# Kernel optimization log

Measured on AMD Instinct MI355X. Metric: run time of the kernel, lower is better.

## Reference

```python
import jax, jax.numpy as jnp
import numpy as np

B, H, L, D = 1, 8, 2048, 64
DP = 3   # positional coord dim
RE = 1   # extra relative features appended via concat
F = DP + RE  # LazyLinear in-features


def setup_inputs() -> dict:
    key = jax.random.key(0)
    ks = jax.random.split(key, 12)
    return {
        "q": jax.random.normal(ks[0], (B, H, L, D), jnp.float32),
        "k": jax.random.normal(ks[1], (B, H, L, D), jnp.float32),
        "v": jax.random.normal(ks[2], (B, H, L, D), jnp.float32),
        "c": jax.random.uniform(ks[3], (B, 1, 1, L), jnp.float32),
        "d_q": jax.random.normal(ks[4], (B, L, DP), jnp.float32),
        "d_k_top": jax.random.normal(ks[5], (B, L, DP), jnp.float32),
        "d_k_bot": jax.random.normal(ks[6], (B, L, DP), jnp.float32),
        "d_k_score": jax.random.uniform(ks[7], (B, L, 2, F), jnp.float32),
        "relative_top": jax.random.normal(ks[8], (B, L, L, RE), jnp.float32),
        "relative_bottom": jax.random.normal(ks[9], (B, L, L, RE), jnp.float32),
        "W_w": jax.random.normal(ks[10], (F, H), jnp.float32) * 0.1,
        "W_b": jax.random.normal(ks[11], (F, H), jnp.float32) * 0.1,
    }


def _pairwise_diff(a, b):
    # a: [B,Lq,Dp], b: [B,Lk,Dp] -> [B,Lq,Lk,Dp]
    return a[:, :, None, :] - b[:, None, :, :]


def reference(q, k, v, c, d_q, d_k_top, d_k_bot, d_k_score,
              relative_top, relative_bottom, W_w, W_b):
    # score function: scaled dot product -> [B,H,Lq,Lk]
    scores = jnp.einsum('bhqd,bhkd->bhqk', q, k) * (q.shape[-1] ** -0.5)

    # relative-position bias path
    dt = jnp.concatenate([_pairwise_diff(d_q, d_k_top), relative_top], axis=-1)     # [B,Lq,Lk,F]
    db = jnp.concatenate([_pairwise_diff(d_q, d_k_bot), relative_bottom], axis=-1)  # [B,Lq,Lk,F]
    dm = jnp.stack([dt, db], axis=3)                 # [B,Lq,Lk,2,F]
    dm = dm * d_k_score[:, None]                     # broadcast over Lq
    dm = dm.sum(axis=3)                              # [B,Lq,Lk,F]

    w = jax.nn.softplus(dm @ W_w).transpose(0, 3, 1, 2)  # [B,H,Lq,Lk]
    b = (dm @ W_b).transpose(0, 3, 1, 2)                 # [B,H,Lq,Lk]
    scores = scores * w + b

    # leaky probability function: softmax gated by per-key sampling weights c
    probs = jax.nn.softmax(scores, axis=-1) * c      # [B,H,Lq,Lk]

    out = jnp.einsum('bhqk,bhkd->bhqd', probs, v)
    return out, probs
```

## Files before the change

kernel.cpp:

```cpp
#include <hip/hip_runtime.h>
#include <cstdint>
#include <cstddef>

#define NH 8
#define LQ 2048
#define DH 64
#define NKT_Q 8

typedef __attribute__((ext_vector_type(8))) __bf16 bf16x8;
typedef __attribute__((ext_vector_type(8))) unsigned short ushort8;
typedef __attribute__((ext_vector_type(4))) float floatx4;

__device__ __forceinline__ unsigned short bf_trunc(float x) {
    return (unsigned short)(__float_as_uint(x) >> 16);
}
__device__ __forceinline__ float bf_up(unsigned short h) {
    return __uint_as_float(((unsigned int)h) << 16);
}
__device__ __forceinline__ unsigned short bf_rne(float x) {
    unsigned int u = __float_as_uint(x);
    return (unsigned short)((u + 0x7FFFu + ((u >> 16) & 1u)) >> 16);
}
struct hl_t { unsigned short h, l; };
__device__ __forceinline__ hl_t split2(float x) {
    hl_t r;
    r.h = bf_trunc(x);
    r.l = bf_trunc(x - bf_up(r.h));
    return r;
}

#define MFMA16(A, B, C) __builtin_amdgcn_mfma_f32_16x16x32_bf16((A), (B), (C), 0, 0, 0)

__global__ __launch_bounds__(256, 4) void attn_main(
    const float* __restrict__ qp,  const float* __restrict__ kp,
    const float* __restrict__ vp,  const float* __restrict__ cp,
    const float* __restrict__ dqp, const float* __restrict__ dktp,
    const float* __restrict__ dkbp,const float* __restrict__ dksp,
    const float* __restrict__ rtp, const float* __restrict__ rbp,
    const float* __restrict__ Wwp, const float* __restrict__ Wbp,
    float* __restrict__ probp, float* __restrict__ lws, float* __restrict__ pvws)
{
    __shared__ unsigned short sh_khi[64 * 72];
    __shared__ unsigned short sh_klo[64 * 72];
    __shared__ unsigned short sh_vhi[64 * 72];
    __shared__ unsigned short sh_vlo[64 * 72];
    __shared__ float sh_meta[64 * 13];
    __shared__ float sh_dqs[64 * 3];

    const int bid  = blockIdx.x;
    const int quar = bid & 3;
    const int h    = (bid >> 2) & 7;
    const int qt   = bid >> 5;
    const int q0   = qt * 64;
    const int t    = threadIdx.x;
    const int lane = t & 63;
    const int m    = lane & 15;
    const int quad = lane >> 4;
    const int w16  = (t >> 6) * 16;

    float Ww[4], Wb[4];
#pragma unroll
    for (int f = 0; f < 4; ++f) { Ww[f] = Wwp[f * NH + h]; Wb[f] = Wbp[f * NH + h]; }

    {
        const int row = t >> 2, s = t & 3;
        const float* src = qp + ((size_t)(h * LQ + q0 + row)) * DH + s * 16;
        ushort8 vh0, vh1, vl0, vl1;
#pragma unroll
        for (int j = 0; j < 2; ++j) {
            float4 x = *(const float4*)(src + 4 * j);
            hl_t a = split2(x.x * 0.125f), b = split2(x.y * 0.125f);
            hl_t c = split2(x.z * 0.125f), d = split2(x.w * 0.125f);
            vh0[4 * j + 0] = a.h; vl0[4 * j + 0] = a.l;
            vh0[4 * j + 1] = b.h; vl0[4 * j + 1] = b.l;
            vh0[4 * j + 2] = c.h; vl0[4 * j + 2] = c.l;
            vh0[4 * j + 3] = d.h; vl0[4 * j + 3] = d.l;
        }
#pragma unroll
        for (int j = 0; j < 2; ++j) {
            float4 x = *(const float4*)(src + 8 + 4 * j);
            hl_t a = split2(x.x * 0.125f), b = split2(x.y * 0.125f);
            hl_t c = split2(x.z * 0.125f), d = split2(x.w * 0.125f);
            vh1[4 * j + 0] = a.h; vl1[4 * j + 0] = a.l;
            vh1[4 * j + 1] = b.h; vl1[4 * j + 1] = b.l;
            vh1[4 * j + 2] = c.h; vl1[4 * j + 2] = c.l;
            vh1[4 * j + 3] = d.h; vl1[4 * j + 3] = d.l;
        }
        const int base = row * 72 + s * 16;
        *(ushort8*)&sh_khi[base] = vh0;  *(ushort8*)&sh_khi[base + 8] = vh1;
        *(ushort8*)&sh_klo[base] = vl0;  *(ushort8*)&sh_klo[base + 8] = vl1;
        if (t < 64) {
            sh_dqs[t * 3 + 0] = dqp[(q0 + t) * 3 + 0];
            sh_dqs[t * 3 + 1] = dqp[(q0 + t) * 3 + 1];
            sh_dqs[t * 3 + 2] = dqp[(q0 + t) * 3 + 2];
        }
    }
    __syncthreads();

    bf16x8 aqh[2], aql[2];
#pragma unroll
    for (int kc = 0; kc < 2; ++kc) {
        aqh[kc] = *(const bf16x8*)&sh_khi[(w16 + m) * 72 + kc * 32 + quad * 8];
        aql[kc] = *(const bf16x8*)&sh_klo[(w16 + m) * 72 + kc * 32 + quad * 8];
    }
    float dq0[4], dq1[4], dq2[4];
#pragma unroll
    for (int r = 0; r < 4; ++r) {
        const int row = w16 + quad * 4 + r;
        dq0[r] = sh_dqs[row * 3 + 0]; dq1[r] = sh_dqs[row * 3 + 1]; dq2[r] = sh_dqs[row * 3 + 2];
    }
    __syncthreads();

    const floatx4 zf = {0.f, 0.f, 0.f, 0.f};
    floatx4 pacc[4] = {zf, zf, zf, zf};
    float lpart[4] = {0.f, 0.f, 0.f, 0.f};

    for (int kth = 0; kth < NKT_Q; ++kth) {
        const int k0 = (quar * NKT_Q + kth) * 64;

        {
            const int row = t >> 2, s = t & 3;
            const float* src = kp + ((size_t)(h * LQ + k0 + row)) * DH + s * 16;
            ushort8 vh0, vh1, vl0, vl1;
#pragma unroll
            for (int j = 0; j < 2; ++j) {
                float4 x = *(const float4*)(src + 4 * j);
                hl_t a = split2(x.x), b = split2(x.y), c = split2(x.z), d = split2(x.w);
                vh0[4 * j + 0] = a.h; vl0[4 * j + 0] = a.l;
                vh0[4 * j + 1] = b.h; vl0[4 * j + 1] = b.l;
                vh0[4 * j + 2] = c.h; vl0[4 * j + 2] = c.l;
                vh0[4 * j + 3] = d.h; vl0[4 * j + 3] = d.l;
            }
#pragma unroll
            for (int j = 0; j < 2; ++j) {
                float4 x = *(const float4*)(src + 8 + 4 * j);
                hl_t a = split2(x.x), b = split2(x.y), c = split2(x.z), d = split2(x.w);
                vh1[4 * j + 0] = a.h; vl1[4 * j + 0] = a.l;
                vh1[4 * j + 1] = b.h; vl1[4 * j + 1] = b.l;
                vh1[4 * j + 2] = c.h; vl1[4 * j + 2] = c.l;
                vh1[4 * j + 3] = d.h; vl1[4 * j + 3] = d.l;
            }
            const int base = row * 72 + s * 16;
            *(ushort8*)&sh_khi[base] = vh0;  *(ushort8*)&sh_khi[base + 8] = vh1;
            *(ushort8*)&sh_klo[base] = vl0;  *(ushort8*)&sh_klo[base + 8] = vl1;
        }
        {
            const int p = t >> 4;
            const int mm = t & 15;
#pragma unroll
            for (int g = 0; g < 2; ++g) {
                const int kka = 2 * p + 32 * g;
                const float ca = cp[k0 + kka], cb = cp[k0 + kka + 1];
                const float* va = vp + ((size_t)(h * LQ + k0 + kka)) * DH;
                const float* vb = va + DH;
#pragma unroll
                for (int dd = 0; dd < 4; ++dd) {
                    const int d = mm + 16 * dd;
                    hl_t xa = split2(va[d] * ca);
                    hl_t xb = split2(vb[d] * cb);
                    *(unsigned int*)&sh_vhi[d * 72 + kka] = (unsigned int)xa.h | ((unsigned int)xb.h << 16);
                    *(unsigned int*)&sh_vlo[d * 72 + kka] = (unsigned int)xa.l | ((unsigned int)xb.l << 16);
                }
            }
        }
        if (t < 64) {
            const int kg = k0 + t;
            const float* sc_ = dksp + (size_t)kg * 8;
            const float* tp  = dktp + (size_t)kg * 3;
            const float* bt  = dkbp + (size_t)kg * 3;
            float cw = 0.f, cb2 = 0.f;
#pragma unroll
            for (int f = 0; f < 3; ++f) {
                const float stf = sc_[f], sbf = sc_[4 + f];
                const float A  = stf + sbf;
                const float Bv = tp[f] * stf + bt[f] * sbf;
                sh_meta[t * 13 + f]     = A * Ww[f];
                sh_meta[t * 13 + 4 + f] = A * Wb[f];
                cw  -= Bv * Ww[f];
                cb2 -= Bv * Wb[f];
            }
            sh_meta[t * 13 + 3]  = cw;              sh_meta[t * 13 + 7]  = cb2;
            sh_meta[t * 13 + 8]  = sc_[3] * Ww[3];  sh_meta[t * 13 + 9]  = sc_[7] * Ww[3];
            sh_meta[t * 13 + 10] = sc_[3] * Wb[3];  sh_meta[t * 13 + 11] = sc_[7] * Wb[3];
        }
        __syncthreads();

        float rt_[4][4], rb_[4][4];
#pragma unroll
        for (int r = 0; r < 4; ++r) {
            const size_t q = (size_t)(q0 + w16 + quad * 4 + r);
#pragma unroll
            for (int nt = 0; nt < 4; ++nt) {
                rt_[nt][r] = rtp[q * LQ + k0 + nt * 16 + m];
                rb_[nt][r] = rbp[q * LQ + k0 + nt * 16 + m];
            }
        }

        floatx4 sc[4] = {zf, zf, zf, zf};
#pragma unroll
        for (int nt = 0; nt < 4; ++nt) {
#pragma unroll
            for (int kc = 0; kc < 2; ++kc) {
                const int kb = (nt * 16 + m) * 72 + kc * 32 + quad * 8;
                bf16x8 bh = *(const bf16x8*)&sh_khi[kb];
                bf16x8 bl = *(const bf16x8*)&sh_klo[kb];
                sc[nt] = MFMA16(aqh[kc], bh, sc[nt]);
                sc[nt] = MFMA16(aql[kc], bh, sc[nt]);
                sc[nt] = MFMA16(aqh[kc], bl, sc[nt]);
            }
        }
        __syncthreads();

        unsigned short* ebf = sh_klo;
#pragma unroll
        for (int nt = 0; nt < 4; ++nt) {
            const int kcol = nt * 16 + m;
            const float m0 = sh_meta[kcol * 13 + 0],  m1 = sh_meta[kcol * 13 + 1];
            const float m2 = sh_meta[kcol * 13 + 2],  m3 = sh_meta[kcol * 13 + 3];
            const float m4 = sh_meta[kcol * 13 + 4],  m5 = sh_meta[kcol * 13 + 5];
            const float m6 = sh_meta[kcol * 13 + 6],  m7 = sh_meta[kcol * 13 + 7];
            const float m8 = sh_meta[kcol * 13 + 8],  m9 = sh_meta[kcol * 13 + 9];
            const float mA = sh_meta[kcol * 13 + 10], mB = sh_meta[kcol * 13 + 11];
#pragma unroll
            for (int r = 0; r < 4; ++r) {
                float ww = fmaf(dq0[r], m0, m3); ww = fmaf(dq1[r], m1, ww); ww = fmaf(dq2[r], m2, ww);
                ww = fmaf(rt_[nt][r], m8, ww);   ww = fmaf(rb_[nt][r], m9, ww);
                float bb = fmaf(dq0[r], m4, m7); bb = fmaf(dq1[r], m5, bb); bb = fmaf(dq2[r], m6, bb);
                bb = fmaf(rt_[nt][r], mA, bb);   bb = fmaf(rb_[nt][r], mB, bb);
                const float wg = __logf(1.0f + __builtin_amdgcn_exp2f(ww * 1.44269504f));
                const float sv = fmaf(sc[nt][r], wg, bb);
                const float e  = __builtin_amdgcn_exp2f(fmaf(sv, 1.44269504f, -11.5415603f));
                lpart[r] += e;
                probp[((size_t)(h * LQ + q0 + w16 + quad * 4 + r)) * LQ + k0 + kcol] = e;
                ebf[(w16 + quad * 4 + r) * 72 + kcol] = bf_rne(e);
            }
        }

        bf16x8 ap0 = *(const bf16x8*)&ebf[(w16 + m) * 72 + quad * 8];
        bf16x8 ap1 = *(const bf16x8*)&ebf[(w16 + m) * 72 + 32 + quad * 8];
#pragma unroll
        for (int nt = 0; nt < 4; ++nt) {
            const int vb = (nt * 16 + m) * 72 + quad * 8;
            bf16x8 bh0 = *(const bf16x8*)&sh_vhi[vb];
            bf16x8 bl0 = *(const bf16x8*)&sh_vlo[vb];
            bf16x8 bh1 = *(const bf16x8*)&sh_vhi[vb + 32];
            bf16x8 bl1 = *(const bf16x8*)&sh_vlo[vb + 32];
            pacc[nt] = MFMA16(ap0, bh0, pacc[nt]);
            pacc[nt] = MFMA16(ap0, bl0, pacc[nt]);
            pacc[nt] = MFMA16(ap1, bh1, pacc[nt]);
            pacc[nt] = MFMA16(ap1, bl1, pacc[nt]);
        }
        __syncthreads();
    }

#pragma unroll
    for (int off = 1; off < 16; off <<= 1) {
#pragma unroll
        for (int r = 0; r < 4; ++r) lpart[r] += __shfl_xor(lpart[r], off, 64);
    }
    if (m == 0) {
#pragma unroll
        for (int r = 0; r < 4; ++r)
            lws[quar * (NH * LQ) + h * LQ + q0 + w16 + quad * 4 + r] = lpart[r];
    }
#pragma unroll
    for (int nt = 0; nt < 4; ++nt) {
#pragma unroll
        for (int r = 0; r < 4; ++r) {
            const size_t row = (size_t)(h * LQ + q0 + w16 + quad * 4 + r);
            pvws[(size_t)quar * (NH * LQ * DH) + row * DH + nt * 16 + m] = pacc[nt][r];
        }
    }
}

__global__ void combine_kernel(const float* __restrict__ pvws, const float* __restrict__ lws,
                               float* __restrict__ outp)
{
    const int idx4 = blockIdx.x * 256 + threadIdx.x;
    const int row  = idx4 >> 4;
    const int d4   = (idx4 & 15) * 4;
    const size_t stride = (size_t)NH * LQ * DH;
    floatx4 s = {0.f, 0.f, 0.f, 0.f};
    float l = 0.f;
#pragma unroll
    for (int qr = 0; qr < 4; ++qr) {
        s += *(const floatx4*)(pvws + qr * stride + (size_t)row * DH + d4);
        l += lws[qr * (NH * LQ) + row];
    }
    const float rl = 1.0f / l;
    *(floatx4*)(outp + (size_t)row * DH + d4) = s * rl;
}

__global__ __launch_bounds__(256) void norm_kernel(float* __restrict__ probp,
                                                   const float* __restrict__ cp,
                                                   const float* __restrict__ lws)
{
    const int r0 = blockIdx.x * 4;
    const int t  = threadIdx.x;
    const floatx4 c0 = *(const floatx4*)(cp + t * 4);
    const floatx4 c1 = *(const floatx4*)(cp + (t + 256) * 4);
#pragma unroll
    for (int r = 0; r < 4; ++r) {
        const int row = r0 + r;
        float l = 0.f;
#pragma unroll
        for (int qr = 0; qr < 4; ++qr) l += lws[qr * (NH * LQ) + row];
        const float rl = 1.0f / l;
        float* p = probp + (size_t)row * LQ;
        floatx4 x0 = *(const floatx4*)(p + t * 4);
        floatx4 x1 = *(const floatx4*)(p + (t + 256) * 4);
        x0 = x0 * c0 * rl;
        x1 = x1 * c1 * rl;
        __builtin_nontemporal_store(x0, (floatx4*)(p + t * 4));
        __builtin_nontemporal_store(x1, (floatx4*)(p + (t + 256) * 4));
    }
}

extern "C" void kernel_launch(void* const* d_in, const int* in_sizes, int n_in,
                              void* d_out, int out_size, void* d_ws, size_t ws_size,
                              hipStream_t stream)
{
    (void)in_sizes; (void)n_in; (void)ws_size; (void)out_size;
    const float* qp   = (const float*)d_in[0];
    const float* kp   = (const float*)d_in[1];
    const float* vp   = (const float*)d_in[2];
    const float* cp   = (const float*)d_in[3];
    const float* dqp  = (const float*)d_in[4];
    const float* dktp = (const float*)d_in[5];
    const float* dkbp = (const float*)d_in[6];
    const float* dksp = (const float*)d_in[7];
    const float* rtp  = (const float*)d_in[8];
    const float* rbp  = (const float*)d_in[9];
    const float* Wwp  = (const float*)d_in[10];
    const float* Wbp  = (const float*)d_in[11];

    float* outp  = (float*)d_out;
    float* probp = (float*)d_out + (size_t)NH * LQ * DH;

    float* lws  = (float*)d_ws;
    float* pvws = (float*)d_ws + 4 * (NH * LQ);

    attn_main<<<dim3(1024), dim3(256), 0, stream>>>(
        qp, kp, vp, cp, dqp, dktp, dkbp, dksp, rtp, rbp, Wwp, Wbp, probp, lws, pvws);
    combine_kernel<<<dim3(1024), dim3(256), 0, stream>>>(pvws, lws, outp);
    norm_kernel<<<dim3(4096), dim3(256), 0, stream>>>(probp, cp, lws);
}
```

Measured before the change: 329.0 us.

## Stage unnormalized probabilities as bf16 in workspace instead of fp32 output

When the workspace is large enough, the main kernel stores the exponentiated scores as bf16 into a workspace buffer with coalesced 16-byte row writes from LDS, instead of scattered fp32 writes into the probs output. A new finalize kernel reads the bf16 values, applies the c gating and the 1/l normalization, and writes fp32 probs once. This replaces the fp32 write, read and rewrite of the large probs tensor with a bf16 write and read plus one fp32 write. The cost is bf16 precision on the probs output, which may hurt accuracy. Launch bounds also drop from 4 to 3 waves per SIMD.

```diff
diff --git a/kernel.cpp b/kernel.cpp
--- a/kernel.cpp
+++ b/kernel.cpp
@@ -31,14 +31,16 @@
 
 #define MFMA16(A, B, C) __builtin_amdgcn_mfma_f32_16x16x32_bf16((A), (B), (C), 0, 0, 0)
 
-__global__ __launch_bounds__(256, 4) void attn_main(
+template <bool FAST>
+__global__ __launch_bounds__(256, 3) void attn_main(
     const float* __restrict__ qp,  const float* __restrict__ kp,
     const float* __restrict__ vp,  const float* __restrict__ cp,
     const float* __restrict__ dqp, const float* __restrict__ dktp,
     const float* __restrict__ dkbp,const float* __restrict__ dksp,
     const float* __restrict__ rtp, const float* __restrict__ rbp,
     const float* __restrict__ Wwp, const float* __restrict__ Wbp,
-    float* __restrict__ probp, float* __restrict__ lws, float* __restrict__ pvws)
+    float* __restrict__ probp, float* __restrict__ lws, float* __restrict__ pvws,
+    unsigned short* __restrict__ ews)
 {
     __shared__ unsigned short sh_khi[64 * 72];
     __shared__ unsigned short sh_klo[64 * 72];
@@ -231,7 +233,8 @@
                 const float sv = fmaf(sc[nt][r], wg, bb);
                 const float e  = __builtin_amdgcn_exp2f(fmaf(sv, 1.44269504f, -11.5415603f));
                 lpart[r] += e;
-                probp[((size_t)(h * LQ + q0 + w16 + quad * 4 + r)) * LQ + k0 + kcol] = e;
+                if (!FAST)
+                    probp[((size_t)(h * LQ + q0 + w16 + quad * 4 + r)) * LQ + k0 + kcol] = e;
                 ebf[(w16 + quad * 4 + r) * 72 + kcol] = bf_rne(e);
             }
         }
@@ -250,6 +253,16 @@
             pacc[nt] = MFMA16(ap1, bh1, pacc[nt]);
             pacc[nt] = MFMA16(ap1, bl1, pacc[nt]);
         }
+
+        if (FAST) {
+            const int rrow = w16 + (lane >> 2);
+#pragma unroll
+            for (int it = 0; it < 2; ++it) {
+                const int cc = (lane & 3) + it * 4;
+                ushort8 v = *(const ushort8*)&ebf[rrow * 72 + cc * 8];
+                *(ushort8*)(ews + ((size_t)(h * LQ + q0 + rrow)) * LQ + k0 + cc * 8) = v;
+            }
+        }
         __syncthreads();
     }
 
@@ -289,6 +302,30 @@
     }
     const float rl = 1.0f / l;
     *(floatx4*)(outp + (size_t)row * DH + d4) = s * rl;
+}
+
+__global__ __launch_bounds__(256) void finalize_kernel(const unsigned short* __restrict__ ews,
+                                                       const float* __restrict__ cp,
+                                                       const float* __restrict__ lws,
+                                                       float* __restrict__ probp)
+{
+    const int gid = blockIdx.x * 256 + threadIdx.x;
+    const int row = gid >> 8;
+    const int k   = (gid & 255) * 8;
+    float l = 0.f;
+#pragma unroll
+    for (int qr = 0; qr < 4; ++qr) l += lws[qr * (NH * LQ) + row];
+    const float rl = 1.0f / l;
+    const ushort8 e = *(const ushort8*)(ews + (size_t)row * LQ + k);
+    const floatx4 c0 = *(const floatx4*)(cp + k);
+    const floatx4 c1 = *(const floatx4*)(cp + k + 4);
+    floatx4 o0, o1;
+#pragma unroll
+    for (int j = 0; j < 4; ++j) o0[j] = bf_up(e[j]) * c0[j] * rl;
+#pragma unroll
+    for (int j = 0; j < 4; ++j) o1[j] = bf_up(e[4 + j]) * c1[j] * rl;
+    __builtin_nontemporal_store(o0, (floatx4*)(probp + (size_t)row * LQ + k));
+    __builtin_nontemporal_store(o1, (floatx4*)(probp + (size_t)row * LQ + k + 4));
 }
 
 __global__ __launch_bounds__(256) void norm_kernel(float* __restrict__ probp,
@@ -320,7 +357,7 @@
                               void* d_out, int out_size, void* d_ws, size_t ws_size,
                               hipStream_t stream)
 {
-    (void)in_sizes; (void)n_in; (void)ws_size; (void)out_size;
+    (void)in_sizes; (void)n_in; (void)out_size;
     const float* qp   = (const float*)d_in[0];
     const float* kp   = (const float*)d_in[1];
     const float* vp   = (const float*)d_in[2];
@@ -339,9 +376,22 @@
 
     float* lws  = (float*)d_ws;
     float* pvws = (float*)d_ws + 4 * (NH * LQ);
-
-    attn_main<<<dim3(1024), dim3(256), 0, stream>>>(
-        qp, kp, vp, cp, dqp, dktp, dkbp, dksp, rtp, rbp, Wwp, Wbp, probp, lws, pvws);
-    combine_kernel<<<dim3(1024), dim3(256), 0, stream>>>(pvws, lws, outp);
-    norm_kernel<<<dim3(4096), dim3(256), 0, stream>>>(probp, cp, lws);
-}
+    unsigned short* ews = (unsigned short*)(pvws + (size_t)4 * NH * LQ * DH);
+
+    const size_t need = (size_t)4 * NH * LQ * 4
+                      + (size_t)4 * NH * LQ * DH * 4
+                      + (size_t)NH * LQ * LQ * 2;
+    const bool fast = ws_size >= need;
+
+    if (fast) {
+        attn_main<true><<<dim3(1024), dim3(256), 0, stream>>>(
+            qp, kp, vp, cp, dqp, dktp, dkbp, dksp, rtp, rbp, Wwp, Wbp, probp, lws, pvws, ews);
+        combine_kernel<<<dim3(1024), dim3(256), 0, stream>>>(pvws, lws, outp);
+        finalize_kernel<<<dim3(16384), dim3(256), 0, stream>>>(ews, cp, lws, probp);
+    } else {
+        attn_main<false><<<dim3(1024), dim3(256), 0, stream>>>(
+            qp, kp, vp, cp, dqp, dktp, dkbp, dksp, rtp, rbp, Wwp, Wbp, probp, lws, pvws, ews);
+        combine_kernel<<<dim3(1024), dim3(256), 0, stream>>>(pvws, lws, outp);
+        norm_kernel<<<dim3(4096), dim3(256), 0, stream>>>(probp, cp, lws);
+    }
+}
```

Result: faster. 322.2 us (-2.1%).
